# Optimization experiments

Measured on AMD Instinct MI355X. Metric: run time of the kernel, lower is better.

## Reference

```python
import jax, jax.numpy as jnp
import numpy as np

N_NODES = 50000
N_EDGES = 800000
NEG_SLOPE = 0.2  # PyG GATConv default negative_slope


def gat_conv(x, W, att_src, att_dst, bias, src, dst, heads, out_ch, concat):
    """PyG GATConv (eval mode, self-loops already appended to src/dst)."""
    n = x.shape[0]
    xh = (x @ W).reshape(n, heads, out_ch)            # [N,H,C]
    a_s = jnp.einsum('nhc,hc->nh', xh, att_src)       # [N,H]
    a_d = jnp.einsum('nhc,hc->nh', xh, att_dst)
    e = a_s[src] + a_d[dst]                           # [E,H]
    e = jnp.where(e > 0, e, NEG_SLOPE * e)            # LeakyReLU
    # segment softmax over incoming edges of each target node (dst)
    m = jax.ops.segment_max(e, dst, num_segments=n)
    e = jnp.exp(e - m[dst])
    denom = jax.ops.segment_sum(e, dst, num_segments=n)
    alpha = e / (denom[dst] + 1e-16)                  # [E,H]
    msg = xh[src] * alpha[:, :, None]                 # [E,H,C]
    out = jax.ops.segment_sum(msg, dst, num_segments=n)  # [N,H,C]
    out = out.reshape(n, heads * out_ch) if concat else out.mean(axis=1)
    return out + bias


def setup_inputs() -> dict:
    key = jax.random.key(0)
    ks = jax.random.split(key, 16)
    x = jax.random.normal(ks[0], (N_NODES, 256), dtype=jnp.float32)
    edge_index = jax.random.randint(ks[1], (2, N_EDGES), 0, N_NODES, dtype=jnp.int32)
    s = 0.05
    return {
        'x': x, 'edge_index': edge_index,
        'W0': jax.random.normal(ks[2], (256, 256), jnp.float32) * s,
        'as0': jax.random.normal(ks[3], (4, 64), jnp.float32) * s,
        'ad0': jax.random.normal(ks[4], (4, 64), jnp.float32) * s,
        'b0': jnp.zeros((256,), jnp.float32),
        'W1': jax.random.normal(ks[5], (256, 256), jnp.float32) * s,
        'as1': jax.random.normal(ks[6], (4, 64), jnp.float32) * s,
        'ad1': jax.random.normal(ks[7], (4, 64), jnp.float32) * s,
        'b1': jnp.zeros((256,), jnp.float32),
        'W2': jax.random.normal(ks[8], (256, 256), jnp.float32) * s,
        'as2': jax.random.normal(ks[9], (1, 256), jnp.float32) * s,
        'ad2': jax.random.normal(ks[10], (1, 256), jnp.float32) * s,
        'b2': jnp.zeros((256,), jnp.float32),
    }


def reference(x, edge_index, W0, as0, ad0, b0, W1, as1, ad1, b1, W2, as2, ad2, b2):
    # PyG GATConv adds self-loops by default
    loops = jnp.arange(x.shape[0], dtype=edge_index.dtype)
    src = jnp.concatenate([edge_index[0], loops])
    dst = jnp.concatenate([edge_index[1], loops])
    h = jax.nn.elu(gat_conv(x, W0, as0, ad0, b0, src, dst, 4, 64, True))
    h = jax.nn.elu(gat_conv(h, W1, as1, ad1, b1, src, dst, 4, 64, True))
    return gat_conv(h, W2, as2, ad2, b2, src, dst, 1, 256, False)
```

## Files before the change

### kernel.cpp

```cpp
#include <hip/hip_runtime.h>
#include <hip/hip_bf16.h>
#include <hip/hip_fp16.h>

#define N_NODES 50000
#define N_EDGES 800000
#define E_TOTAL (N_EDGES + N_NODES)

typedef _Float16 f16x8 __attribute__((ext_vector_type(8)));
typedef _Float16 f16x4 __attribute__((ext_vector_type(4)));
typedef float f32x4 __attribute__((ext_vector_type(4)));

__device__ __forceinline__ void gl_lds16(const _Float16* g, _Float16* l) {
  __builtin_amdgcn_global_load_lds(
      (const __attribute__((address_space(1))) unsigned int*)g,
      (__attribute__((address_space(3))) unsigned int*)l, 16, 0, 0);
}

#define XCAST_BLK (N_NODES * 256 / 8 / 256)
#define DEG_BLK ((E_TOTAL + 255) / 256)
__global__ __launch_bounds__(256) void prep_kernel(
    const float* __restrict__ W0, const float* __restrict__ W1,
    const float* __restrict__ W2, const float* __restrict__ x,
    const int* __restrict__ ei, _Float16* __restrict__ WT0,
    _Float16* __restrict__ WT1, _Float16* __restrict__ WT2,
    _Float16* __restrict__ X16, int* __restrict__ deg) {
  __shared__ float tile[32][33];
  const int bid = blockIdx.x;
  if (bid < 192) {
    const float* W = (bid < 64) ? W0 : (bid < 128) ? W1 : W2;
    _Float16* WT = (bid < 64) ? WT0 : (bid < 128) ? WT1 : WT2;
    const int sub = bid & 63;
    const int bx = (sub & 7) * 32, by = (sub >> 3) * 32;
    const int tx = threadIdx.x & 31, ty = threadIdx.x >> 5;
#pragma unroll
    for (int i = 0; i < 32; i += 8)
      tile[ty + i][tx] = W[(size_t)(by + ty + i) * 256 + bx + tx];
    __syncthreads();
#pragma unroll
    for (int i = 0; i < 32; i += 8)
      WT[(size_t)(bx + ty + i) * 256 + by + tx] = (_Float16)tile[tx][ty + i];
  } else if (bid < 192 + XCAST_BLK) {
    size_t i = ((size_t)(bid - 192) * 256 + threadIdx.x) * 8;
    float4 u0 = *(const float4*)(x + i);
    float4 u1 = *(const float4*)(x + i + 4);
    f16x8 v;
    v[0] = (_Float16)u0.x; v[1] = (_Float16)u0.y;
    v[2] = (_Float16)u0.z; v[3] = (_Float16)u0.w;
    v[4] = (_Float16)u1.x; v[5] = (_Float16)u1.y;
    v[6] = (_Float16)u1.z; v[7] = (_Float16)u1.w;
    *(f16x8*)(X16 + i) = v;
  } else {
    int e = (bid - 192 - XCAST_BLK) * 256 + threadIdx.x;
    if (e < E_TOTAL) {
      int d = (e < N_EDGES) ? ei[N_EDGES + e] : (e - N_EDGES);
      atomicAdd(&deg[d], 1);
    }
  }
}

__global__ __launch_bounds__(1024) void scan_kernel(const int* __restrict__ deg,
                                                    int* __restrict__ row_ptr) {
  __shared__ int wsum[16];
  __shared__ int carry_sh;
  const int t = threadIdx.x, lane = t & 63, wv = t >> 6;
  if (t == 0) carry_sh = 0;
  __syncthreads();
  const int ITEMS = 8;
  for (int base = 0; base < N_NODES; base += 1024 * ITEMS) {
    int i0 = base + t * ITEMS;
    int v[ITEMS];
    int s = 0;
#pragma unroll
    for (int j = 0; j < ITEMS; j++) {
      v[j] = (i0 + j < N_NODES) ? deg[i0 + j] : 0;
      s += v[j];
    }
    int sc = s;
#pragma unroll
    for (int off = 1; off < 64; off <<= 1) {
      int u = __shfl_up(sc, off, 64);
      if (lane >= off) sc += u;
    }
    if (lane == 63) wsum[wv] = sc;
    __syncthreads();
    if (wv == 0 && lane < 16) {
      int ws = wsum[lane];
#pragma unroll
      for (int off = 1; off < 16; off <<= 1) {
        int u = __shfl_up(ws, off, 64);
        if (lane >= off) ws += u;
      }
      wsum[lane] = ws;
    }
    __syncthreads();
    int wbase = carry_sh + (wv ? wsum[wv - 1] : 0);
    int run = wbase + sc - s;
#pragma unroll
    for (int j = 0; j < ITEMS; j++) {
      if (i0 + j < N_NODES) row_ptr[i0 + j] = run;
      run += v[j];
    }
    __syncthreads();
    if (t == 0) carry_sh += wsum[15];
    __syncthreads();
  }
  if (t == 0) row_ptr[N_NODES] = carry_sh;
}

__global__ __launch_bounds__(256) void scatter_kernel(const int* __restrict__ ei,
                                                      const int* __restrict__ row_ptr,
                                                      int* __restrict__ cursor,
                                                      int* __restrict__ csr_src) {
  int e = blockIdx.x * 256 + threadIdx.x;
  if (e >= E_TOTAL) return;
  int s, d;
  if (e < N_EDGES) {
    s = ei[e];
    d = ei[N_EDGES + e];
  } else {
    s = d = e - N_EDGES;
  }
  int pos = row_ptr[d] + atomicAdd(&cursor[d], 1);
  csr_src[pos] = s;
}

template <int H>
__global__ __launch_bounds__(256) void gemm_att(
    const _Float16* __restrict__ A, const _Float16* __restrict__ WT,
    const float* __restrict__ att_s, const float* __restrict__ att_d,
    _Float16* __restrict__ C, float* __restrict__ a_s, float* __restrict__ a_d,
    int M) {
  __shared__ _Float16 As[2][64 * 32];
  __shared__ _Float16 Bs[2][256 * 32];
  const int t = threadIdx.x, lane = t & 63, w = t >> 6;
  const int wr = w & 1, wc = w >> 1;
  const int row0 = blockIdx.x * 64;
  const int fr = lane & 15, fg = lane >> 4;
  const int srow = lane >> 2, sk = (lane & 3) * 8;

  f32x4 acc[2][8] = {};
  int cur = 0;

#define STAGE(buf, k0)                                                        \
  do {                                                                        \
    gl_lds16(A + (size_t)(row0 + w * 16 + srow) * 256 + (k0) + sk,            \
             &As[buf][w * 512]);                                              \
    gl_lds16(WT + (size_t)(w * 64 + srow) * 256 + (k0) + sk,                  \
             &Bs[buf][w * 2048]);                                             \
    gl_lds16(WT + (size_t)(w * 64 + 16 + srow) * 256 + (k0) + sk,             \
             &Bs[buf][w * 2048 + 512]);                                       \
    gl_lds16(WT + (size_t)(w * 64 + 32 + srow) * 256 + (k0) + sk,             \
             &Bs[buf][w * 2048 + 1024]);                                      \
    gl_lds16(WT + (size_t)(w * 64 + 48 + srow) * 256 + (k0) + sk,             \
             &Bs[buf][w * 2048 + 1536]);                                      \
  } while (0)

  STAGE(0, 0);
  __syncthreads();

  for (int kt = 0; kt < 8; kt++) {
    if (kt < 7) STAGE(cur ^ 1, (kt + 1) * 32);
    f16x8 af[2], bf[8];
#pragma unroll
    for (int mi = 0; mi < 2; mi++)
      af[mi] = *(const f16x8*)&As[cur][(wr * 32 + mi * 16 + fr) * 32 + fg * 8];
#pragma unroll
    for (int ni = 0; ni < 8; ni++)
      bf[ni] = *(const f16x8*)&Bs[cur][(wc * 128 + ni * 16 + fr) * 32 + fg * 8];
#pragma unroll
    for (int mi = 0; mi < 2; mi++)
#pragma unroll
      for (int ni = 0; ni < 8; ni++)
        acc[mi][ni] = __builtin_amdgcn_mfma_f32_16x16x32_f16(af[mi], bf[ni], acc[mi][ni], 0, 0, 0);
    __syncthreads();
    cur ^= 1;
  }
#undef STAGE

  float as_c[8], ad_c[8];
#pragma unroll
  for (int ni = 0; ni < 8; ni++) {
    int c = wc * 128 + ni * 16 + fr;
    as_c[ni] = att_s[c];
    ad_c[ni] = att_d[c];
  }

#pragma unroll
  for (int mi = 0; mi < 2; mi++) {
#pragma unroll
    for (int reg = 0; reg < 4; reg++) {
      const int r = row0 + wr * 32 + mi * 16 + fg * 4 + reg;
      const bool valid = r < M;
      if (valid) {
#pragma unroll
        for (int ni = 0; ni < 8; ni++)
          C[(size_t)r * 256 + wc * 128 + ni * 16 + fr] = (_Float16)acc[mi][ni][reg];
      }
      float s0 = 0.f, s1 = 0.f, d0 = 0.f, d1 = 0.f;
#pragma unroll
      for (int ni = 0; ni < 4; ni++) {
        s0 = fmaf(acc[mi][ni][reg], as_c[ni], s0);
        d0 = fmaf(acc[mi][ni][reg], ad_c[ni], d0);
        s1 = fmaf(acc[mi][ni + 4][reg], as_c[ni + 4], s1);
        d1 = fmaf(acc[mi][ni + 4][reg], ad_c[ni + 4], d1);
      }
#pragma unroll
      for (int off = 1; off < 16; off <<= 1) {
        s0 += __shfl_xor(s0, off, 64);
        d0 += __shfl_xor(d0, off, 64);
        s1 += __shfl_xor(s1, off, 64);
        d1 += __shfl_xor(d1, off, 64);
      }
      if constexpr (H == 4) {
        if (fr == 0 && valid) {
          a_s[(size_t)r * 4 + wc * 2 + 0] = s0;
          a_s[(size_t)r * 4 + wc * 2 + 1] = s1;
          a_d[(size_t)r * 4 + wc * 2 + 0] = d0;
          a_d[(size_t)r * 4 + wc * 2 + 1] = d1;
        }
      } else {
        if (fr == 0) {
          float* L = (float*)As;
          L[(r - row0) * 4 + wc * 2 + 0] = s0 + s1;
          L[(r - row0) * 4 + wc * 2 + 1] = d0 + d1;
        }
      }
    }
  }
  if constexpr (H == 1) {
    __syncthreads();
    float* L = (float*)As;
    if (t < 64 && row0 + t < M) {
      a_s[row0 + t] = L[t * 4 + 0] + L[t * 4 + 2];
      a_d[row0 + t] = L[t * 4 + 1] + L[t * 4 + 3];
    }
  }
}

template <int H, bool ELU_OUT, bool OUT_F16>
__global__ __launch_bounds__(256, 8) void aggregate_kernel(
    const _Float16* __restrict__ XH16, const float* __restrict__ a_s,
    const float* __restrict__ a_d, const int* __restrict__ row_ptr,
    const int* __restrict__ csr_src, const float* __restrict__ bias,
    void* __restrict__ outp) {
  const int t = threadIdx.x;
  const int lane = t & 63, w = t >> 6;
  const int d = blockIdx.x * 4 + w;
  const int e0 = row_ptr[d];
  const int deg = row_ptr[d + 1] - e0;
  const int li = lane & 15;
  const int h4 = (H == 4) ? (lane >> 4) : 0;
  const float adv = (H == 4) ? a_d[(size_t)d * 4 + h4] : a_d[d];

  float dnp = 0.f;
  float acc0 = 0.f, acc1 = 0.f, acc2 = 0.f, acc3 = 0.f;
  for (int base = 0; base < deg; base += 16) {
    const int cnt = min(16, deg - base);
    int s_cur = 0;
    float p = 0.f;
    if (li < cnt) {
      s_cur = csr_src[e0 + base + li];
      float e = ((H == 4) ? a_s[(size_t)s_cur * 4 + h4] : a_s[s_cur]) + adv;
      e = e > 0.f ? e : 0.2f * e;
      p = __expf(e);
    }
    dnp += p;
#define GAT_BODY(j)                                                           \
  {                                                                           \
    int sj = __builtin_amdgcn_readfirstlane(__shfl(s_cur, (j), 64));          \
    float alj = __shfl(p, (lane & 48) + (j), 64);                             \
    f16x4 raw = *(const f16x4*)(XH16 + (size_t)sj * 256 + lane * 4);          \
    acc0 = fmaf(alj, (float)raw[0], acc0);                                    \
    acc1 = fmaf(alj, (float)raw[1], acc1);                                    \
    acc2 = fmaf(alj, (float)raw[2], acc2);                                    \
    acc3 = fmaf(alj, (float)raw[3], acc3);                                    \
  }
    if (cnt == 16) {
#pragma unroll
      for (int j = 0; j < 16; j++) GAT_BODY(j)
    } else {
      for (int j = 0; j < cnt; j++) GAT_BODY(j)
    }
#undef GAT_BODY
  }
#pragma unroll
  for (int off = 1; off < 16; off <<= 1) dnp += __shfl_xor(dnp, off, 64);
  const float inv = 1.f / (dnp + 1e-16f);

  float4 bv = *(const float4*)&bias[lane * 4];
  float v0 = fmaf(acc0, inv, bv.x), v1 = fmaf(acc1, inv, bv.y);
  float v2 = fmaf(acc2, inv, bv.z), v3 = fmaf(acc3, inv, bv.w);
  if constexpr (ELU_OUT) {
    v0 = v0 > 0.f ? v0 : (__expf(v0) - 1.f);
    v1 = v1 > 0.f ? v1 : (__expf(v1) - 1.f);
    v2 = v2 > 0.f ? v2 : (__expf(v2) - 1.f);
    v3 = v3 > 0.f ? v3 : (__expf(v3) - 1.f);
  }
  if constexpr (OUT_F16) {
    _Float16* out = (_Float16*)outp;
    f16x4 ov;
    ov[0] = (_Float16)v0; ov[1] = (_Float16)v1;
    ov[2] = (_Float16)v2; ov[3] = (_Float16)v3;
    *(f16x4*)(out + (size_t)d * 256 + lane * 4) = ov;
  } else {
    float* out = (float*)outp;
    *(float4*)(out + (size_t)d * 256 + lane * 4) = make_float4(v0, v1, v2, v3);
  }
}

extern "C" void kernel_launch(void* const* d_in, const int* in_sizes, int n_in,
                              void* d_out, int out_size, void* d_ws, size_t ws_size,
                              hipStream_t stream) {
  const float* x = (const float*)d_in[0];
  const int* ei = (const int*)d_in[1];
  const float* W0 = (const float*)d_in[2];
  const float* as0 = (const float*)d_in[3];
  const float* ad0 = (const float*)d_in[4];
  const float* b0 = (const float*)d_in[5];
  const float* W1 = (const float*)d_in[6];
  const float* as1 = (const float*)d_in[7];
  const float* ad1 = (const float*)d_in[8];
  const float* b1 = (const float*)d_in[9];
  const float* W2 = (const float*)d_in[10];
  const float* as2 = (const float*)d_in[11];
  const float* ad2 = (const float*)d_in[12];
  const float* b2 = (const float*)d_in[13];
  float* out = (float*)d_out;

  char* p = (char*)d_ws;
  _Float16* XH16 = (_Float16*)p;
  p += (size_t)N_NODES * 256 * 2;
  _Float16* H16 = (_Float16*)p;
  p += (size_t)N_NODES * 256 * 2;
  _Float16* WT0 = (_Float16*)p;
  p += 256 * 256 * 2;
  _Float16* WT1 = (_Float16*)p;
  p += 256 * 256 * 2;
  _Float16* WT2 = (_Float16*)p;
  p += 256 * 256 * 2;
  float* a_s = (float*)p;
  p += (size_t)N_NODES * 4 * 4;
  float* a_d = (float*)p;
  p += (size_t)N_NODES * 4 * 4;
  int* row_ptr = (int*)p;
  p += 200064;
  int* deg = (int*)p;
  p += (size_t)N_NODES * 4;
  int* cursor = (int*)p;
  p += (size_t)N_NODES * 4;
  int* csr_src = (int*)p;
  p += (size_t)E_TOTAL * 4;

  hipMemsetAsync(deg, 0, (size_t)N_NODES * 4 * 2, stream);

  prep_kernel<<<192 + XCAST_BLK + DEG_BLK, 256, 0, stream>>>(
      W0, W1, W2, x, ei, WT0, WT1, WT2, H16, deg);

  scan_kernel<<<1, 1024, 0, stream>>>(deg, row_ptr);
  scatter_kernel<<<(E_TOTAL + 255) / 256, 256, 0, stream>>>(ei, row_ptr, cursor, csr_src);

  const int ggrid = (N_NODES + 63) / 64;
  const int ngrid = N_NODES / 4;

  gemm_att<4><<<ggrid, 256, 0, stream>>>(H16, WT0, as0, ad0, XH16, a_s, a_d, N_NODES);
  aggregate_kernel<4, true, true><<<ngrid, 256, 0, stream>>>(XH16, a_s, a_d, row_ptr, csr_src, b0, H16);
  gemm_att<4><<<ggrid, 256, 0, stream>>>(H16, WT1, as1, ad1, XH16, a_s, a_d, N_NODES);
  aggregate_kernel<4, true, true><<<ngrid, 256, 0, stream>>>(XH16, a_s, a_d, row_ptr, csr_src, b1, H16);
  gemm_att<1><<<ggrid, 256, 0, stream>>>(H16, WT2, as2, ad2, XH16, a_s, a_d, N_NODES);
  aggregate_kernel<1, false, false><<<ngrid, 256, 0, stream>>>(XH16, a_s, a_d, row_ptr, csr_src, b2, out);
}
```

Measured before the change: 396.8 us.

## Fuse scan, scatter, GEMMs and aggregations into persistent grid-barrier megakernel

Replaces the scan, scatter, three GEMM and three aggregation launches with one persistent kernel of 512 blocks. Phases are separated by software grid barriers built on atomic counters. The degree scan runs on one block while the other blocks compute the first-layer GEMM, which takes the serial single-block scan off the critical path and removes per-launch gaps. The GEMM tile is reworked for 8 waves per 512-thread block, and aggregation handles 8 nodes per block iteration. In exchange, correctness depends on all blocks being co-resident. The barrier spins and the tighter register budget could hurt the aggregation and GEMM phases.

After: 760.4 us. 1.92x slower.

```diff
diff --git a/kernel.cpp b/kernel.cpp
--- a/kernel.cpp
+++ b/kernel.cpp
@@ -5,6 +5,8 @@
 #define N_NODES 50000
 #define N_EDGES 800000
 #define E_TOTAL (N_EDGES + N_NODES)
+#define NB 512
+#define NTILES 782
 
 typedef _Float16 f16x8 __attribute__((ext_vector_type(8)));
 typedef _Float16 f16x4 __attribute__((ext_vector_type(4)));
@@ -14,6 +16,18 @@
   __builtin_amdgcn_global_load_lds(
       (const __attribute__((address_space(1))) unsigned int*)g,
       (__attribute__((address_space(3))) unsigned int*)l, 16, 0, 0);
+}
+
+__device__ __forceinline__ void gbar(unsigned* ctr) {
+  __syncthreads();
+  if (threadIdx.x == 0) {
+    __hip_atomic_fetch_add(ctr, 1u, __ATOMIC_ACQ_REL, __HIP_MEMORY_SCOPE_AGENT);
+    while (__hip_atomic_load(ctr, __ATOMIC_RELAXED, __HIP_MEMORY_SCOPE_AGENT) <
+           (unsigned)NB)
+      __builtin_amdgcn_s_sleep(2);
+    (void)__hip_atomic_load(ctr, __ATOMIC_ACQUIRE, __HIP_MEMORY_SCOPE_AGENT);
+  }
+  __syncthreads();
 }
 
 #define XCAST_BLK (N_NODES * 256 / 8 / 256)
@@ -58,101 +72,30 @@
   }
 }
 
-__global__ __launch_bounds__(1024) void scan_kernel(const int* __restrict__ deg,
-                                                    int* __restrict__ row_ptr) {
-  __shared__ int wsum[16];
-  __shared__ int carry_sh;
-  const int t = threadIdx.x, lane = t & 63, wv = t >> 6;
-  if (t == 0) carry_sh = 0;
-  __syncthreads();
-  const int ITEMS = 8;
-  for (int base = 0; base < N_NODES; base += 1024 * ITEMS) {
-    int i0 = base + t * ITEMS;
-    int v[ITEMS];
-    int s = 0;
-#pragma unroll
-    for (int j = 0; j < ITEMS; j++) {
-      v[j] = (i0 + j < N_NODES) ? deg[i0 + j] : 0;
-      s += v[j];
-    }
-    int sc = s;
-#pragma unroll
-    for (int off = 1; off < 64; off <<= 1) {
-      int u = __shfl_up(sc, off, 64);
-      if (lane >= off) sc += u;
-    }
-    if (lane == 63) wsum[wv] = sc;
-    __syncthreads();
-    if (wv == 0 && lane < 16) {
-      int ws = wsum[lane];
-#pragma unroll
-      for (int off = 1; off < 16; off <<= 1) {
-        int u = __shfl_up(ws, off, 64);
-        if (lane >= off) ws += u;
-      }
-      wsum[lane] = ws;
-    }
-    __syncthreads();
-    int wbase = carry_sh + (wv ? wsum[wv - 1] : 0);
-    int run = wbase + sc - s;
-#pragma unroll
-    for (int j = 0; j < ITEMS; j++) {
-      if (i0 + j < N_NODES) row_ptr[i0 + j] = run;
-      run += v[j];
-    }
-    __syncthreads();
-    if (t == 0) carry_sh += wsum[15];
-    __syncthreads();
-  }
-  if (t == 0) row_ptr[N_NODES] = carry_sh;
-}
-
-__global__ __launch_bounds__(256) void scatter_kernel(const int* __restrict__ ei,
-                                                      const int* __restrict__ row_ptr,
-                                                      int* __restrict__ cursor,
-                                                      int* __restrict__ csr_src) {
-  int e = blockIdx.x * 256 + threadIdx.x;
-  if (e >= E_TOTAL) return;
-  int s, d;
-  if (e < N_EDGES) {
-    s = ei[e];
-    d = ei[N_EDGES + e];
-  } else {
-    s = d = e - N_EDGES;
-  }
-  int pos = row_ptr[d] + atomicAdd(&cursor[d], 1);
-  csr_src[pos] = s;
-}
-
 template <int H>
-__global__ __launch_bounds__(256) void gemm_att(
+__device__ __forceinline__ void gemm_tile(
     const _Float16* __restrict__ A, const _Float16* __restrict__ WT,
     const float* __restrict__ att_s, const float* __restrict__ att_d,
     _Float16* __restrict__ C, float* __restrict__ a_s, float* __restrict__ a_d,
-    int M) {
-  __shared__ _Float16 As[2][64 * 32];
-  __shared__ _Float16 Bs[2][256 * 32];
-  const int t = threadIdx.x, lane = t & 63, w = t >> 6;
+    int row0, _Float16 (&As)[2][2048], _Float16 (&Bs)[2][8192], int t,
+    int lane, int w) {
   const int wr = w & 1, wc = w >> 1;
-  const int row0 = blockIdx.x * 64;
   const int fr = lane & 15, fg = lane >> 4;
   const int srow = lane >> 2, sk = (lane & 3) * 8;
 
-  f32x4 acc[2][8] = {};
+  f32x4 acc[2][4] = {};
   int cur = 0;
 
-#define STAGE(buf, k0)                                                        \
-  do {                                                                        \
-    gl_lds16(A + (size_t)(row0 + w * 16 + srow) * 256 + (k0) + sk,            \
-             &As[buf][w * 512]);                                              \
-    gl_lds16(WT + (size_t)(w * 64 + srow) * 256 + (k0) + sk,                  \
-             &Bs[buf][w * 2048]);                                             \
-    gl_lds16(WT + (size_t)(w * 64 + 16 + srow) * 256 + (k0) + sk,             \
-             &Bs[buf][w * 2048 + 512]);                                       \
-    gl_lds16(WT + (size_t)(w * 64 + 32 + srow) * 256 + (k0) + sk,             \
-             &Bs[buf][w * 2048 + 1024]);                                      \
-    gl_lds16(WT + (size_t)(w * 64 + 48 + srow) * 256 + (k0) + sk,             \
-             &Bs[buf][w * 2048 + 1536]);                                      \
+#define STAGE(buf, k0)                                                         \
+  do {                                                                         \
+    for (int s = w; s < 20; s += 8) {                                          \
+      if (s < 4)                                                               \
+        gl_lds16(A + (size_t)(row0 + s * 16 + srow) * 256 + (k0) + sk,         \
+                 &As[buf][s * 512]);                                           \
+      else                                                                     \
+        gl_lds16(WT + (size_t)((s - 4) * 16 + srow) * 256 + (k0) + sk,         \
+                 &Bs[buf][(s - 4) * 512]);                                     \
+    }                                                                          \
   } while (0)
 
   STAGE(0, 0);
@@ -160,27 +103,27 @@
 
   for (int kt = 0; kt < 8; kt++) {
     if (kt < 7) STAGE(cur ^ 1, (kt + 1) * 32);
-    f16x8 af[2], bf[8];
+    f16x8 af[2], bf[4];
 #pragma unroll
     for (int mi = 0; mi < 2; mi++)
       af[mi] = *(const f16x8*)&As[cur][(wr * 32 + mi * 16 + fr) * 32 + fg * 8];
 #pragma unroll
-    for (int ni = 0; ni < 8; ni++)
-      bf[ni] = *(const f16x8*)&Bs[cur][(wc * 128 + ni * 16 + fr) * 32 + fg * 8];
+    for (int ni = 0; ni < 4; ni++)
+      bf[ni] = *(const f16x8*)&Bs[cur][(wc * 64 + ni * 16 + fr) * 32 + fg * 8];
 #pragma unroll
     for (int mi = 0; mi < 2; mi++)
 #pragma unroll
-      for (int ni = 0; ni < 8; ni++)
+      for (int ni = 0; ni < 4; ni++)
         acc[mi][ni] = __builtin_amdgcn_mfma_f32_16x16x32_f16(af[mi], bf[ni], acc[mi][ni], 0, 0, 0);
     __syncthreads();
     cur ^= 1;
   }
 #undef STAGE
 
-  float as_c[8], ad_c[8];
-#pragma unroll
-  for (int ni = 0; ni < 8; ni++) {
-    int c = wc * 128 + ni * 16 + fr;
+  float as_c[4], ad_c[4];
+#pragma unroll
+  for (int ni = 0; ni < 4; ni++) {
+    int c = wc * 64 + ni * 16 + fr;
     as_c[ni] = att_s[c];
     ad_c[ni] = att_d[c];
   }
@@ -190,39 +133,33 @@
 #pragma unroll
     for (int reg = 0; reg < 4; reg++) {
       const int r = row0 + wr * 32 + mi * 16 + fg * 4 + reg;
-      const bool valid = r < M;
+      const bool valid = r < N_NODES;
       if (valid) {
 #pragma unroll
-        for (int ni = 0; ni < 8; ni++)
-          C[(size_t)r * 256 + wc * 128 + ni * 16 + fr] = (_Float16)acc[mi][ni][reg];
-      }
-      float s0 = 0.f, s1 = 0.f, d0 = 0.f, d1 = 0.f;
+        for (int ni = 0; ni < 4; ni++)
+          C[(size_t)r * 256 + wc * 64 + ni * 16 + fr] = (_Float16)acc[mi][ni][reg];
+      }
+      float s0 = 0.f, d0 = 0.f;
 #pragma unroll
       for (int ni = 0; ni < 4; ni++) {
         s0 = fmaf(acc[mi][ni][reg], as_c[ni], s0);
         d0 = fmaf(acc[mi][ni][reg], ad_c[ni], d0);
-        s1 = fmaf(acc[mi][ni + 4][reg], as_c[ni + 4], s1);
-        d1 = fmaf(acc[mi][ni + 4][reg], ad_c[ni + 4], d1);
       }
 #pragma unroll
       for (int off = 1; off < 16; off <<= 1) {
         s0 += __shfl_xor(s0, off, 64);
         d0 += __shfl_xor(d0, off, 64);
-        s1 += __shfl_xor(s1, off, 64);
-        d1 += __shfl_xor(d1, off, 64);
       }
       if constexpr (H == 4) {
         if (fr == 0 && valid) {
-          a_s[(size_t)r * 4 + wc * 2 + 0] = s0;
-          a_s[(size_t)r * 4 + wc * 2 + 1] = s1;
-          a_d[(size_t)r * 4 + wc * 2 + 0] = d0;
-          a_d[(size_t)r * 4 + wc * 2 + 1] = d1;
+          a_s[(size_t)r * 4 + wc] = s0;
+          a_d[(size_t)r * 4 + wc] = d0;
         }
       } else {
         if (fr == 0) {
           float* L = (float*)As;
-          L[(r - row0) * 4 + wc * 2 + 0] = s0 + s1;
-          L[(r - row0) * 4 + wc * 2 + 1] = d0 + d1;
+          L[(r - row0) * 4 + wc] = s0;
+          L[256 + (r - row0) * 4 + wc] = d0;
         }
       }
     }
@@ -230,22 +167,20 @@
   if constexpr (H == 1) {
     __syncthreads();
     float* L = (float*)As;
-    if (t < 64 && row0 + t < M) {
-      a_s[row0 + t] = L[t * 4 + 0] + L[t * 4 + 2];
-      a_d[row0 + t] = L[t * 4 + 1] + L[t * 4 + 3];
+    if (t < 64 && row0 + t < N_NODES) {
+      a_s[row0 + t] = L[t * 4 + 0] + L[t * 4 + 1] + L[t * 4 + 2] + L[t * 4 + 3];
+      a_d[row0 + t] = L[256 + t * 4 + 0] + L[256 + t * 4 + 1] +
+                      L[256 + t * 4 + 2] + L[256 + t * 4 + 3];
     }
   }
 }
 
 template <int H, bool ELU_OUT, bool OUT_F16>
-__global__ __launch_bounds__(256, 8) void aggregate_kernel(
+__device__ __forceinline__ void agg_node(
     const _Float16* __restrict__ XH16, const float* __restrict__ a_s,
     const float* __restrict__ a_d, const int* __restrict__ row_ptr,
     const int* __restrict__ csr_src, const float* __restrict__ bias,
-    void* __restrict__ outp) {
-  const int t = threadIdx.x;
-  const int lane = t & 63, w = t >> 6;
-  const int d = blockIdx.x * 4 + w;
+    void* __restrict__ outp, int d, int lane) {
   const int e0 = row_ptr[d];
   const int deg = row_ptr[d + 1] - e0;
   const int li = lane & 15;
@@ -306,6 +241,113 @@
     float* out = (float*)outp;
     *(float4*)(out + (size_t)d * 256 + lane * 4) = make_float4(v0, v1, v2, v3);
   }
+}
+
+__global__ __launch_bounds__(512, 4) void mega_kernel(
+    const int* __restrict__ ei, const int* __restrict__ deg,
+    int* __restrict__ row_ptr, int* __restrict__ cursor,
+    int* __restrict__ csr_src, unsigned* __restrict__ barctr,
+    const _Float16* __restrict__ X16, _Float16* __restrict__ XH16,
+    _Float16* __restrict__ H16, const _Float16* __restrict__ WT0,
+    const _Float16* __restrict__ WT1, const _Float16* __restrict__ WT2,
+    const float* __restrict__ as0, const float* __restrict__ ad0,
+    const float* __restrict__ b0, const float* __restrict__ as1,
+    const float* __restrict__ ad1, const float* __restrict__ b1,
+    const float* __restrict__ as2, const float* __restrict__ ad2,
+    const float* __restrict__ b2, float* __restrict__ a_s,
+    float* __restrict__ a_d, float* __restrict__ out) {
+  __shared__ _Float16 As[2][2048];
+  __shared__ _Float16 Bs[2][8192];
+  const int t = threadIdx.x, lane = t & 63, w = t >> 6, bid = blockIdx.x;
+
+  if (bid == NB - 1) {
+    __shared__ int wsum[8];
+    __shared__ int carry_sh;
+    if (t == 0) carry_sh = 0;
+    __syncthreads();
+    const int ITEMS = 16;
+    for (int base = 0; base < N_NODES; base += 512 * ITEMS) {
+      int i0 = base + t * ITEMS;
+      int v[ITEMS];
+      int s = 0;
+#pragma unroll
+      for (int j = 0; j < ITEMS; j++) {
+        v[j] = (i0 + j < N_NODES) ? deg[i0 + j] : 0;
+        s += v[j];
+      }
+      int sc = s;
+#pragma unroll
+      for (int off = 1; off < 64; off <<= 1) {
+        int u = __shfl_up(sc, off, 64);
+        if (lane >= off) sc += u;
+      }
+      if (lane == 63) wsum[w] = sc;
+      __syncthreads();
+      if (w == 0 && lane < 8) {
+        int ws = wsum[lane];
+#pragma unroll
+        for (int off = 1; off < 8; off <<= 1) {
+          int u = __shfl_up(ws, off, 64);
+          if (lane >= off) ws += u;
+        }
+        wsum[lane] = ws;
+      }
+      __syncthreads();
+      int wbase = carry_sh + (w ? wsum[w - 1] : 0);
+      int run = wbase + sc - s;
+#pragma unroll
+      for (int j = 0; j < ITEMS; j++) {
+        if (i0 + j < N_NODES) row_ptr[i0 + j] = run;
+        run += v[j];
+      }
+      __syncthreads();
+      if (t == 0) carry_sh += wsum[7];
+      __syncthreads();
+    }
+    if (t == 0) row_ptr[N_NODES] = carry_sh;
+  } else {
+    for (int tile = bid; tile < NTILES; tile += NB - 1) {
+      __syncthreads();
+      gemm_tile<4>(X16, WT0, as0, ad0, XH16, a_s, a_d, tile * 64, As, Bs, t, lane, w);
+    }
+  }
+  gbar(&barctr[0]);
+
+  for (int e = bid * 512 + t; e < E_TOTAL; e += NB * 512) {
+    int s, d;
+    if (e < N_EDGES) {
+      s = ei[e];
+      d = ei[N_EDGES + e];
+    } else {
+      s = d = e - N_EDGES;
+    }
+    int pos = row_ptr[d] + atomicAdd(&cursor[d], 1);
+    csr_src[pos] = s;
+  }
+  gbar(&barctr[1]);
+
+  for (int g = bid; g < N_NODES / 8; g += NB)
+    agg_node<4, true, true>(XH16, a_s, a_d, row_ptr, csr_src, b0, H16, g * 8 + w, lane);
+  gbar(&barctr[2]);
+
+  for (int tile = bid; tile < NTILES; tile += NB) {
+    __syncthreads();
+    gemm_tile<4>(H16, WT1, as1, ad1, XH16, a_s, a_d, tile * 64, As, Bs, t, lane, w);
+  }
+  gbar(&barctr[3]);
+
+  for (int g = bid; g < N_NODES / 8; g += NB)
+    agg_node<4, true, true>(XH16, a_s, a_d, row_ptr, csr_src, b1, H16, g * 8 + w, lane);
+  gbar(&barctr[4]);
+
+  for (int tile = bid; tile < NTILES; tile += NB) {
+    __syncthreads();
+    gemm_tile<1>(H16, WT2, as2, ad2, XH16, a_s, a_d, tile * 64, As, Bs, t, lane, w);
+  }
+  gbar(&barctr[5]);
+
+  for (int g = bid; g < N_NODES / 8; g += NB)
+    agg_node<1, false, false>(XH16, a_s, a_d, row_ptr, csr_src, b2, out, g * 8 + w, lane);
 }
 
 extern "C" void kernel_launch(void* const* d_in, const int* in_sizes, int n_in,
@@ -348,24 +390,17 @@
   p += (size_t)N_NODES * 4;
   int* cursor = (int*)p;
   p += (size_t)N_NODES * 4;
+  unsigned* barctr = (unsigned*)p;
+  p += 64;
   int* csr_src = (int*)p;
   p += (size_t)E_TOTAL * 4;
 
-  hipMemsetAsync(deg, 0, (size_t)N_NODES * 4 * 2, stream);
+  hipMemsetAsync(deg, 0, (size_t)N_NODES * 4 * 2 + 64, stream);
 
   prep_kernel<<<192 + XCAST_BLK + DEG_BLK, 256, 0, stream>>>(
       W0, W1, W2, x, ei, WT0, WT1, WT2, H16, deg);
 
-  scan_kernel<<<1, 1024, 0, stream>>>(deg, row_ptr);
-  scatter_kernel<<<(E_TOTAL + 255) / 256, 256, 0, stream>>>(ei, row_ptr, cursor, csr_src);
-
-  const int ggrid = (N_NODES + 63) / 64;
-  const int ngrid = N_NODES / 4;
-
-  gemm_att<4><<<ggrid, 256, 0, stream>>>(H16, WT0, as0, ad0, XH16, a_s, a_d, N_NODES);
-  aggregate_kernel<4, true, true><<<ngrid, 256, 0, stream>>>(XH16, a_s, a_d, row_ptr, csr_src, b0, H16);
-  gemm_att<4><<<ggrid, 256, 0, stream>>>(H16, WT1, as1, ad1, XH16, a_s, a_d, N_NODES);
-  aggregate_kernel<4, true, true><<<ngrid, 256, 0, stream>>>(XH16, a_s, a_d, row_ptr, csr_src, b1, H16);
-  gemm_att<1><<<ggrid, 256, 0, stream>>>(H16, WT2, as2, ad2, XH16, a_s, a_d, N_NODES);
-  aggregate_kernel<1, false, false><<<ngrid, 256, 0, stream>>>(XH16, a_s, a_d, row_ptr, csr_src, b2, out);
-}
+  mega_kernel<<<NB, 512, 0, stream>>>(
+      ei, deg, row_ptr, cursor, csr_src, barctr, H16, XH16, H16, WT0, WT1, WT2,
+      as0, ad0, b0, as1, ad1, b1, as2, ad2, b2, a_s, a_d, out);
+}
```
